# Optimization experiments

Hardware: AMD Instinct MI355X
Metric: run time of the kernel (lower is better)

The kernel has to match this reference:

```python
import jax, jax.numpy as jnp
import numpy as np
from jax import lax

EPS = 1e-5  # BatchNorm eps (torch default)


def _bn_relu_conv3x3_s2(x, bn_w, bn_b, bn_m, bn_v, w, b):
    # eval-mode BatchNorm2d -> ReLU -> conv3x3 stride 2 pad 1 (NCHW)
    inv = bn_w / jnp.sqrt(bn_v + EPS)
    y = x * inv[None, :, None, None] + (bn_b - bn_m * inv)[None, :, None, None]
    y = jax.nn.relu(y)
    y = lax.conv_general_dilated(y, w, window_strides=(2, 2),
                                 padding=((1, 1), (1, 1)),
                                 dimension_numbers=("NCHW", "OIHW", "NCHW"))
    return y + b[None, :, None, None]


def _avgpool2x2(x):
    B, C, H, W = x.shape
    return x.reshape(B, C, H // 2, 2, W // 2, 2).mean(axis=(3, 5))


def setup_inputs() -> dict:
    key = jax.random.key(0)
    ks = jax.random.split(key, 24)
    C, C3 = 128, 128 // 3
    d = {"x": jax.random.normal(ks[0], (8, C, 96, 96), jnp.float32)}
    for i, p in enumerate(["f", "g", "h"]):
        base = 1 + i * 6
        d[p + "_bn_w"] = jax.random.uniform(ks[base], (C,), jnp.float32, 0.5, 1.5)
        d[p + "_bn_b"] = jax.random.normal(ks[base + 1], (C,), jnp.float32) * 0.1
        d[p + "_bn_m"] = jax.random.normal(ks[base + 2], (C,), jnp.float32) * 0.1
        d[p + "_bn_v"] = jax.random.uniform(ks[base + 3], (C,), jnp.float32, 0.5, 1.5)
        d[p + "_w"] = jax.random.normal(ks[base + 4], (C, C, 3, 3), jnp.float32) * (1.0 / np.sqrt(9 * C))
        d[p + "_b"] = jax.random.normal(ks[base + 5], (C,), jnp.float32) * 0.01
    d["se_cw"] = jax.random.normal(ks[19], (C3, 2 * C), jnp.float32) * (1.0 / np.sqrt(2 * C))
    d["se_cb"] = jax.random.normal(ks[20], (C3,), jnp.float32) * 0.01
    d["se_uw"] = jax.random.normal(ks[21], (C, C3), jnp.float32) * (1.0 / np.sqrt(C3))
    d["se_ub"] = jax.random.normal(ks[22], (C,), jnp.float32) * 0.01
    d["gamma"] = jax.random.normal(ks[23], (1,), jnp.float32) * 0.5
    return d


def reference(x, f_bn_w, f_bn_b, f_bn_m, f_bn_v, f_w, f_b,
              g_bn_w, g_bn_b, g_bn_m, g_bn_v, g_w, g_b,
              h_bn_w, h_bn_b, h_bn_m, h_bn_v, h_w, h_b,
              se_cw, se_cb, se_uw, se_ub, gamma):
    B, C, H, W = x.shape
    left = _avgpool2x2(x)  # isPrimary=False branch -> [B,C,H/2,W/2]

    f = _bn_relu_conv3x3_s2(x, f_bn_w, f_bn_b, f_bn_m, f_bn_v, f_w, f_b)
    g = _bn_relu_conv3x3_s2(x, g_bn_w, g_bn_b, g_bn_m, g_bn_v, g_w, g_b)
    h = _bn_relu_conv3x3_s2(x, h_bn_w, h_bn_b, h_bn_m, h_bn_v, h_w, h_b)

    Ho, Wo = f.shape[2], f.shape[3]
    N = Ho * Wo
    ff = f.reshape(B, C, N)
    gg = g.reshape(B, C, N)
    hh = h.reshape(B, C, N)

    # s = softmax over last axis of f^T g : [B, N, N]
    scores = jnp.einsum("bcn,bcm->bnm", ff, gg)
    attn = jax.nn.softmax(scores, axis=2)
    s = jnp.einsum("bcn,bnm->bcm", hh, attn).reshape(B, C, Ho, Wo)
    s = gamma[0] * s

    # CompetitiveSE: global-avg x and s -> concat(2C) -> ReLU/1x1(C//3) -> ReLU/1x1(C)
    wx = x.mean(axis=(2, 3))          # [B, C]
    ws = s.mean(axis=(2, 3))          # [B, C]
    wcat = jnp.concatenate([wx, ws], axis=1)  # [B, 2C]
    se = jax.nn.relu(wcat) @ se_cw.T + se_cb
    se = jax.nn.relu(se) @ se_uw.T + se_ub    # [B, C]

    return (left + s) * (1.0 + se[:, :, None, None])
```

## Files before the change

kernel.cpp:

```cpp
#include <hip/hip_runtime.h>
#include <hip/hip_bf16.h>

#define B_   8
#define C_   128
#define H_   96
#define W_   96
#define HP_  98
#define HO_  48
#define N_   2304
#define K_CONV 1152
#define PLANE_IN  9216
#define TOT_OUT (B_*C_*N_)

typedef __attribute__((ext_vector_type(8))) short          s16x8;
typedef __attribute__((ext_vector_type(8))) unsigned short u16x8;
typedef __attribute__((ext_vector_type(4))) unsigned short u16x4;
typedef __attribute__((ext_vector_type(4))) float          f32x4;

#define SW(row, q)   (((row) << 6) + ((((q) ^ (((row) >> 1) & 3))) << 4))
#define SW8(row, q)  (((row) << 7) + ((((q) ^ ((row) & 7))) << 4))
#define SW16(row, q) (((row) << 8) + ((((q) ^ ((row) & 15))) << 4))

__device__ __forceinline__ ushort f2bf(float f) {
  __hip_bfloat16 h = __float2bfloat16(f);
  return *reinterpret_cast<ushort*>(&h);
}

__device__ __forceinline__ float block_reduce_sum_256(float v) {
  #pragma unroll
  for (int o = 32; o > 0; o >>= 1) v += __shfl_down(v, o, 64);
  __shared__ float r[4];
  int lane = threadIdx.x & 63, wv = threadIdx.x >> 6;
  if (lane == 0) r[wv] = v;
  __syncthreads();
  float s = 0.f;
  if (threadIdx.x == 0) s = r[0] + r[1] + r[2] + r[3];
  __syncthreads();
  return s;
}

__global__ void k_prep(const float* __restrict__ w0, const float* __restrict__ b0,
                       const float* __restrict__ m0, const float* __restrict__ v0,
                       const float* __restrict__ w1, const float* __restrict__ b1,
                       const float* __restrict__ m1, const float* __restrict__ v1,
                       const float* __restrict__ w2, const float* __restrict__ b2,
                       const float* __restrict__ m2, const float* __restrict__ v2,
                       float* __restrict__ inv, float* __restrict__ beta) {
  int p = blockIdx.x, c = threadIdx.x;
  const float* w = (p == 0 ? w0 : p == 1 ? w1 : w2);
  const float* bb = (p == 0 ? b0 : p == 1 ? b1 : b2);
  const float* m = (p == 0 ? m0 : p == 1 ? m1 : m2);
  const float* v = (p == 0 ? v0 : p == 1 ? v1 : v2);
  if (c < C_) {
    float iv = w[c] / sqrtf(v[c] + 1e-5f);
    inv[p * 128 + c] = iv;
    beta[p * 128 + c] = bb[c] - m[c] * iv;
  }
}

__global__ __launch_bounds__(256) void k_prep_w(const float* __restrict__ w0,
                                                const float* __restrict__ w1,
                                                const float* __restrict__ w2,
                                                ushort* __restrict__ o0,
                                                ushort* __restrict__ o1,
                                                ushort* __restrict__ o2) {
  int p = blockIdx.y;
  const float* w = (p == 0 ? w0 : p == 1 ? w1 : w2);
  ushort* wb = (p == 0 ? o0 : p == 1 ? o1 : o2);
  int id = blockIdx.x * 256 + threadIdx.x;
  if (id >= C_ * K_CONV) return;
  int co = id / K_CONV, rem = id - co * K_CONV;
  int tap = rem >> 7, ci = rem & 127;
  wb[id] = f2bf(w[co * K_CONV + ci * 9 + tap]);
}

__global__ __launch_bounds__(256) void k_prep_y(const float* __restrict__ x,
                                                const float* __restrict__ pinv,
                                                const float* __restrict__ pbeta,
                                                ushort* __restrict__ y0,
                                                ushort* __restrict__ y1,
                                                ushort* __restrict__ y2) {
  const int h1 = blockIdx.x, b = blockIdx.y, t = threadIdx.x;
  ushort* ys[3] = {y0 + (size_t)b * HP_ * HP_ * C_,
                   y1 + (size_t)b * HP_ * HP_ * C_,
                   y2 + (size_t)b * HP_ * HP_ * C_};
  u16x8 zer = (u16x8)0;
  if (h1 == 0 || h1 == HP_ - 1) {
    for (int p = 0; p < 3; ++p)
      for (int g = t; g < HP_ * C_ / 8; g += 256)
        *(u16x8*)(ys[p] + (size_t)h1 * HP_ * C_ + g * 8) = zer;
    return;
  }
  __shared__ float xs[128][97];
  const int h = h1 - 1;
  const float* xb = x + (size_t)b * C_ * PLANE_IN + h * W_;
  for (int id = t; id < 128 * 24; id += 256) {
    int ci = id / 24, w4 = id - ci * 24;
    float4 v = *(const float4*)(xb + (size_t)ci * PLANE_IN + w4 * 4);
    xs[ci][w4 * 4 + 0] = v.x; xs[ci][w4 * 4 + 1] = v.y;
    xs[ci][w4 * 4 + 2] = v.z; xs[ci][w4 * 4 + 3] = v.w;
  }
  __syncthreads();
  if (t < 32) {
    int side = t >> 4, cg = t & 15;
    for (int p = 0; p < 3; ++p)
      *(u16x8*)(ys[p] + ((size_t)h1 * HP_ + (side ? HP_ - 1 : 0)) * C_ + cg * 8) = zer;
  }
  for (int p = 0; p < 3; ++p) {
    const float* inv = pinv + p * 128;
    const float* bet = pbeta + p * 128;
    for (int g = t; g < 96 * 16; g += 256) {
      int wdx = g >> 4, cg = g & 15;
      u16x8 o;
      #pragma unroll
      for (int k = 0; k < 8; ++k) {
        int ci = cg * 8 + k;
        o[k] = f2bf(fmaxf(xs[ci][wdx] * inv[ci] + bet[ci], 0.f));
      }
      *(u16x8*)(ys[p] + ((size_t)h1 * HP_ + (wdx + 1)) * C_ + cg * 8) = o;
    }
  }
}

__global__ __launch_bounds__(256) void k_meanx(const float* __restrict__ x,
                                               float* __restrict__ wcat) {
  int bc = blockIdx.x;
  const float* p = x + (size_t)bc * PLANE_IN;
  float s = 0.f;
  for (int i = threadIdx.x; i < PLANE_IN; i += 256) s += p[i];
  s = block_reduce_sum_256(s);
  if (threadIdx.x == 0) {
    int b = bc >> 7, c = bc & 127;
    wcat[b * 256 + c] = fmaxf(s * (1.f / PLANE_IN), 0.f);
  }
}

__global__ __launch_bounds__(256) void k_conv3(
    const ushort* __restrict__ y0, const ushort* __restrict__ y1, const ushort* __restrict__ y2,
    const ushort* __restrict__ w0, const ushort* __restrict__ w1, const ushort* __restrict__ w2,
    const float* __restrict__ bi0, const float* __restrict__ bi1, const float* __restrict__ bi2,
    ushort* __restrict__ fo, ushort* __restrict__ go, ushort* __restrict__ ho) {
  __shared__ __align__(16) char smem[16384];
  char* As = smem;
  char* Bs = smem + 8192;
  const int br = blockIdx.y, b = blockIdx.z, n0 = blockIdx.x * 64;
  const int t = threadIdx.x, l = t & 63, w = t >> 6;
  const ushort* yb = (br == 0 ? y0 : br == 1 ? y1 : y2) + (size_t)b * HP_ * HP_ * C_;
  const ushort* wb = (br == 0 ? w0 : br == 1 ? w1 : w2);
  const float* bias = (br == 0 ? bi0 : br == 1 ? bi1 : bi2);
  const int pos = t >> 2, q = t & 3;
  const int n_glob = n0 + pos;
  const int oh = n_glob / HO_, ow = n_glob - oh * HO_;
  const int mh = (w & 1) * 64, nh = (w >> 1) * 32;
  f32x4 acc[4][2];
  #pragma unroll
  for (int i = 0; i < 4; ++i)
    #pragma unroll
    for (int j = 0; j < 2; ++j) acc[i][j] = (f32x4)0.f;

  for (int k0 = 0; k0 < K_CONV; k0 += 32) {
    int tap = k0 >> 7, ci0 = k0 & 127;
    int kh = tap / 3, kw = tap - kh * 3;
    #pragma unroll
    for (int g2 = 0; g2 < 2; ++g2) {
      int g = t + g2 * 256, row = g >> 2, qq = g & 3;
      u16x8 d = *(const u16x8*)(wb + row * K_CONV + k0 + qq * 8);
      *(u16x8*)(As + SW(row, qq)) = d;
    }
    {
      int h1 = 2 * oh + kh, w1 = 2 * ow + kw;
      u16x8 d = *(const u16x8*)(yb + ((size_t)h1 * HP_ + w1) * C_ + ci0 + q * 8);
      *(u16x8*)(Bs + SW(pos, q)) = d;
    }
    __syncthreads();
    s16x8 af[4], bf[2];
    #pragma unroll
    for (int i = 0; i < 4; ++i) {
      int r = mh + i * 16 + (l & 15);
      af[i] = *(const s16x8*)(As + SW(r, (l >> 4)));
    }
    #pragma unroll
    for (int j = 0; j < 2; ++j) {
      int r = nh + j * 16 + (l & 15);
      bf[j] = *(const s16x8*)(Bs + SW(r, (l >> 4)));
    }
    #pragma unroll
    for (int i = 0; i < 4; ++i)
      #pragma unroll
      for (int j = 0; j < 2; ++j)
        acc[i][j] = __builtin_amdgcn_mfma_f32_16x16x32_bf16(af[i], bf[j], acc[i][j], 0, 0, 0);
    __syncthreads();
  }

  if (br < 2) {
    ushort* out = (br == 0) ? fo : go;
    ushort* tb = (ushort*)smem;
    #pragma unroll
    for (int i = 0; i < 4; ++i) {
      int co4 = mh + i * 16 + (l >> 4) * 4;
      float4 bi = *(const float4*)&bias[co4];
      float bia[4] = {bi.x, bi.y, bi.z, bi.w};
      #pragma unroll
      for (int j = 0; j < 2; ++j) {
        int pp = nh + j * 16 + (l & 15);
        #pragma unroll
        for (int r = 0; r < 4; ++r)
          tb[pp * 128 + co4 + r] = f2bf(acc[i][j][r] + bia[r]);
      }
    }
    __syncthreads();
    #pragma unroll
    for (int it = 0; it < 4; ++it) {
      int g = t + it * 256;
      int row = g >> 4, gg = g & 15;
      u16x8 d = *(const u16x8*)(tb + row * 128 + gg * 8);
      *(u16x8*)(out + ((size_t)b * N_ + n0 + row) * C_ + gg * 8) = d;
    }
  } else {
    ushort* tb = (ushort*)smem;
    #pragma unroll
    for (int i = 0; i < 4; ++i) {
      int co4 = mh + i * 16 + (l >> 4) * 4;
      float4 bi = *(const float4*)&bias[co4];
      float bia[4] = {bi.x, bi.y, bi.z, bi.w};
      #pragma unroll
      for (int j = 0; j < 2; ++j) {
        int pp = nh + j * 16 + (l & 15);
        #pragma unroll
        for (int r = 0; r < 4; ++r)
          tb[(co4 + r) * 64 + pp] = f2bf(acc[i][j][r] + bia[r]);
      }
    }
    __syncthreads();
    for (int g = t; g < 1024; g += 256) {
      int co = g >> 3, off2 = (g & 7) * 8;
      u16x8 d = *(const u16x8*)(tb + co * 64 + off2);
      *(u16x8*)(ho + ((size_t)b * C_ + co) * N_ + n0 + off2) = d;
    }
  }
}

__global__ __launch_bounds__(256) void k_stats(const ushort* __restrict__ f,
                                               const ushort* __restrict__ g,
                                               float2* __restrict__ pstats) {
  __shared__ __align__(16) char smem[32768];
  char* fs = smem;
  char* gs = smem + 16384;
  const int blk = blockIdx.x;
  const int b = blk & 7, t2 = blk >> 3;
  const int n0 = (t2 % 36) * 64, mz = t2 / 36;
  const int t = threadIdx.x, l = t & 63, w = t >> 6, lo = l & 15, quad = l >> 4;
  const ushort* fb = f + (size_t)b * N_ * C_;
  const ushort* gb = g + (size_t)b * N_ * C_;
  #pragma unroll
  for (int it = 0; it < 4; ++it) {
    int G = t + it * 256, row = G >> 4, g16 = G & 15;
    *(u16x8*)(fs + SW16(row, g16)) = *(const u16x8*)(fb + (size_t)(n0 + row) * C_ + g16 * 8);
  }
  __syncthreads();
  s16x8 af[4];
  #pragma unroll
  for (int ks = 0; ks < 4; ++ks)
    af[ks] = *(const s16x8*)(fs + SW16(w * 16 + lo, ks * 4 + quad));
  float mloc[4], lloc[4];
  #pragma unroll
  for (int r = 0; r < 4; ++r) { mloc[r] = -1e30f; lloc[r] = 0.f; }
  const int m_beg = mz * 576;

  for (int i9 = 0; i9 < 9; ++i9) {
    int m0 = m_beg + i9 * 64;
    __syncthreads();
    #pragma unroll
    for (int it = 0; it < 4; ++it) {
      int G = t + it * 256, row = G >> 4, g16 = G & 15;
      *(u16x8*)(gs + SW16(row, g16)) = *(const u16x8*)(gb + (size_t)(m0 + row) * C_ + g16 * 8);
    }
    __syncthreads();
    f32x4 acc[4];
    #pragma unroll
    for (int j = 0; j < 4; ++j) acc[j] = (f32x4)0.f;
    #pragma unroll
    for (int ks = 0; ks < 4; ++ks)
      #pragma unroll
      for (int j = 0; j < 4; ++j) {
        s16x8 bf = *(const s16x8*)(gs + SW16(j * 16 + lo, ks * 4 + quad));
        acc[j] = __builtin_amdgcn_mfma_f32_16x16x32_bf16(af[ks], bf, acc[j], 0, 0, 0);
      }
    #pragma unroll
    for (int r = 0; r < 4; ++r) {
      float vmax = fmaxf(fmaxf(acc[0][r], acc[1][r]), fmaxf(acc[2][r], acc[3][r]));
      float mn = fmaxf(mloc[r], vmax);
      lloc[r] = lloc[r] * __expf(mloc[r] - mn) +
                __expf(acc[0][r] - mn) + __expf(acc[1][r] - mn) +
                __expf(acc[2][r] - mn) + __expf(acc[3][r] - mn);
      mloc[r] = mn;
    }
  }
  #pragma unroll
  for (int r = 0; r < 4; ++r) {
    #pragma unroll
    for (int o = 1; o < 16; o <<= 1) {
      float mo = __shfl_xor(mloc[r], o, 64);
      float lo2 = __shfl_xor(lloc[r], o, 64);
      float mn = fmaxf(mloc[r], mo);
      lloc[r] = lloc[r] * __expf(mloc[r] - mn) + lo2 * __expf(mo - mn);
      mloc[r] = mn;
    }
  }
  if (lo == 0) {
    #pragma unroll
    for (int r = 0; r < 4; ++r)
      pstats[((size_t)mz * B_ + b) * N_ + n0 + w * 16 + quad * 4 + r] =
          make_float2(mloc[r], lloc[r]);
  }
}

__global__ __launch_bounds__(256) void k_stats_red(const float2* __restrict__ p,
                                                   float2* __restrict__ stats) {
  int idx = blockIdx.x * 256 + threadIdx.x;
  if (idx >= B_ * N_) return;
  float mx = -1e30f, ls = 0.f;
  #pragma unroll
  for (int z = 0; z < 4; ++z) {
    float2 s = p[(size_t)z * B_ * N_ + idx];
    float mn = fmaxf(mx, s.x);
    ls = ls * __expf(mx - mn) + s.y * __expf(s.x - mn);
    mx = mn;
  }
  stats[idx] = make_float2(mx, ls);
}

__global__ __launch_bounds__(256) void k_attn_out(const ushort* __restrict__ f,
                                                  const ushort* __restrict__ g,
                                                  const ushort* __restrict__ h,
                                                  const float2* __restrict__ stats,
                                                  float* __restrict__ spart) {
  __shared__ __align__(16) char smem[35072];
  char* gs = smem;
  char* pTb = smem + 16384;
  const int blk = blockIdx.x;
  const int b = blk & 7, t2 = blk >> 3;
  const int m0 = (t2 % 36) * 64, nz = t2 / 36;
  const int t = threadIdx.x, l = t & 63, w = t >> 6, lo = l & 15, quad = l >> 4;
  const ushort* fb = f + (size_t)b * N_ * C_;
  const ushort* gb = g + (size_t)b * N_ * C_;
  const ushort* hb = h + (size_t)b * C_ * N_;
  const float2* stb = stats + (size_t)b * N_;
  #pragma unroll
  for (int it = 0; it < 4; ++it) {
    int G = t + it * 256, row = G >> 4, g16 = G & 15;
    *(u16x8*)(gs + SW16(row, g16)) = *(const u16x8*)(gb + (size_t)(m0 + row) * C_ + g16 * 8);
  }
  __syncthreads();
  f32x4 accs[2][4];
  #pragma unroll
  for (int i = 0; i < 2; ++i)
    #pragma unroll
    for (int j = 0; j < 4; ++j) accs[i][j] = (f32x4)0.f;
  const int n_beg = nz * 576;

  for (int i9 = 0; i9 < 9; ++i9) {
    int nb = n_beg + i9 * 64;
    char* pT = pTb + ((i9 & 1) << 13);
    s16x8 af[4], ah[2][2];
    #pragma unroll
    for (int ks = 0; ks < 4; ++ks)
      af[ks] = *(const s16x8*)(fb + (size_t)(nb + w * 16 + lo) * C_ + (ks * 4 + quad) * 8);
    #pragma unroll
    for (int i = 0; i < 2; ++i)
      #pragma unroll
      for (int ks = 0; ks < 2; ++ks)
        ah[i][ks] = *(const s16x8*)(hb + (size_t)((2 * w + i) * 16 + lo) * N_ + nb + (ks * 4 + quad) * 8);
    f32x4 sc[4];
    #pragma unroll
    for (int j = 0; j < 4; ++j) sc[j] = (f32x4)0.f;
    #pragma unroll
    for (int ks = 0; ks < 4; ++ks)
      #pragma unroll
      for (int j = 0; j < 4; ++j) {
        s16x8 bg = *(const s16x8*)(gs + SW16(j * 16 + lo, ks * 4 + quad));
        sc[j] = __builtin_amdgcn_mfma_f32_16x16x32_bf16(af[ks], bg, sc[j], 0, 0, 0);
      }
    float mxr[4], ilr[4];
    #pragma unroll
    for (int r = 0; r < 4; ++r) {
      float2 st = stb[nb + w * 16 + quad * 4 + r];
      mxr[r] = st.x; ilr[r] = 1.f / st.y;
    }
    const int nl = w * 16 + quad * 4;
    #pragma unroll
    for (int j = 0; j < 4; ++j) {
      u16x4 pv;
      #pragma unroll
      for (int r = 0; r < 4; ++r)
        pv[r] = f2bf(__expf(sc[j][r] - mxr[r]) * ilr[r]);
      *(u16x4*)(pT + SW8(j * 16 + lo, nl >> 3) + (nl & 7) * 2) = pv;
    }
    __syncthreads();
    #pragma unroll
    for (int ks = 0; ks < 2; ++ks)
      #pragma unroll
      for (int j = 0; j < 4; ++j) {
        s16x8 bp = *(const s16x8*)(pT + SW8(j * 16 + lo, ks * 4 + quad));
        accs[0][j] = __builtin_amdgcn_mfma_f32_16x16x32_bf16(ah[0][ks], bp, accs[0][j], 0, 0, 0);
        accs[1][j] = __builtin_amdgcn_mfma_f32_16x16x32_bf16(ah[1][ks], bp, accs[1][j], 0, 0, 0);
      }
  }
  __syncthreads();
  float* ss = (float*)smem;
  #pragma unroll
  for (int i = 0; i < 2; ++i) {
    int c0 = (2 * w + i) * 16 + quad * 4;
    #pragma unroll
    for (int j = 0; j < 4; ++j) {
      int m = j * 16 + lo;
      #pragma unroll
      for (int r = 0; r < 4; ++r)
        ss[(c0 + r) * 68 + m] = accs[i][j][r];
    }
  }
  __syncthreads();
  float* outp = spart + (size_t)nz * TOT_OUT + (size_t)b * C_ * N_ + m0;
  #pragma unroll
  for (int it = 0; it < 8; ++it) {
    int idx = t + it * 256;
    int c = idx >> 4, mq = idx & 15;
    float4 v = *(const float4*)&ss[c * 68 + mq * 4];
    *(float4*)&outp[(size_t)c * N_ + mq * 4] = v;
  }
}

__global__ __launch_bounds__(256) void k_sred(const float* __restrict__ spart,
                                              const float* __restrict__ gammap,
                                              float* __restrict__ sbuf) {
  int idx = blockIdx.x * 256 + threadIdx.x;
  if (idx >= TOT_OUT) return;
  float s = spart[idx] + spart[(size_t)TOT_OUT + idx] +
            spart[2 * (size_t)TOT_OUT + idx] + spart[3 * (size_t)TOT_OUT + idx];
  sbuf[idx] = gammap[0] * s;
}

__global__ __launch_bounds__(256) void k_means(const float* __restrict__ s,
                                               float* __restrict__ wcat) {
  int bc = blockIdx.x;
  const float* p = s + (size_t)bc * N_;
  float sm = 0.f;
  for (int i = threadIdx.x; i < N_; i += 256) sm += p[i];
  sm = block_reduce_sum_256(sm);
  if (threadIdx.x == 0) {
    int b = bc >> 7, c = bc & 127;
    wcat[b * 256 + 128 + c] = fmaxf(sm * (1.f / N_), 0.f);
  }
}

__global__ __launch_bounds__(128) void k_se(const float* __restrict__ wcat,
                                            const float* __restrict__ cw,
                                            const float* __restrict__ cb,
                                            const float* __restrict__ uw,
                                            const float* __restrict__ ub,
                                            float* __restrict__ se) {
  const int b = blockIdx.x, t = threadIdx.x;
  __shared__ float wc[256];
  __shared__ float s1[42];
  wc[t] = wcat[b * 256 + t];
  wc[128 + t] = wcat[b * 256 + 128 + t];
  __syncthreads();
  if (t < 42) {
    float a = cb[t];
    const float* r = cw + (size_t)t * 256;
    for (int k = 0; k < 256; ++k) a += wc[k] * r[k];
    s1[t] = fmaxf(a, 0.f);
  }
  __syncthreads();
  {
    float a = ub[t];
    const float* r = uw + (size_t)t * 42;
    for (int j = 0; j < 42; ++j) a += s1[j] * r[j];
    se[b * 128 + t] = a;
  }
}

__global__ __launch_bounds__(256) void k_final(const float* __restrict__ x,
                                               const float* __restrict__ s,
                                               const float* __restrict__ se,
                                               float* __restrict__ out) {
  int idx = blockIdx.x * 256 + threadIdx.x;
  if (idx >= TOT_OUT) return;
  int m  = idx % N_;
  int bc = idx / N_;
  int oh = m / HO_, ow = m - oh * HO_;
  const float* xp = x + (size_t)bc * PLANE_IN;
  int ih = oh * 2, iw = ow * 2;
  float l = 0.25f * (xp[ih * W_ + iw] + xp[ih * W_ + iw + 1] +
                     xp[(ih + 1) * W_ + iw] + xp[(ih + 1) * W_ + iw + 1]);
  out[idx] = (l + s[idx]) * (1.f + se[bc]);
}

extern "C" void kernel_launch(void* const* d_in, const int* in_sizes, int n_in,
                              void* d_out, int out_size, void* d_ws, size_t ws_size,
                              hipStream_t stream) {
  (void)in_sizes; (void)n_in; (void)out_size; (void)ws_size;
  const float* x    = (const float*)d_in[0];
  const float* bnw[3] = {(const float*)d_in[1],  (const float*)d_in[7],  (const float*)d_in[13]};
  const float* bnb[3] = {(const float*)d_in[2],  (const float*)d_in[8],  (const float*)d_in[14]};
  const float* bnm[3] = {(const float*)d_in[3],  (const float*)d_in[9],  (const float*)d_in[15]};
  const float* bnv[3] = {(const float*)d_in[4],  (const float*)d_in[10], (const float*)d_in[16]};
  const float* cw_[3] = {(const float*)d_in[5],  (const float*)d_in[11], (const float*)d_in[17]};
  const float* cbb[3] = {(const float*)d_in[6],  (const float*)d_in[12], (const float*)d_in[18]};
  const float* secw = (const float*)d_in[19];
  const float* secb = (const float*)d_in[20];
  const float* seuw = (const float*)d_in[21];
  const float* seub = (const float*)d_in[22];
  const float* gamma = (const float*)d_in[23];
  float* out = (float*)d_out;

  char* ws = (char*)d_ws;
  size_t off = 0;
  auto alloc = [&](size_t bytes) -> char* {
    char* p = ws + off;
    off = (off + bytes + 255) & ~(size_t)255;
    return p;
  };
  ushort* yp[3];
  for (int p = 0; p < 3; ++p) yp[p] = (ushort*)alloc((size_t)B_ * HP_ * HP_ * C_ * 2);
  ushort* wb[3];
  for (int p = 0; p < 3; ++p) wb[p] = (ushort*)alloc((size_t)C_ * K_CONV * 2);
  ushort* fbuf = (ushort*)alloc((size_t)B_ * N_ * C_ * 2);
  ushort* gbuf = (ushort*)alloc((size_t)B_ * N_ * C_ * 2);
  ushort* hbuf = (ushort*)alloc((size_t)B_ * C_ * N_ * 2);
  float2* pstats = (float2*)alloc((size_t)4 * B_ * N_ * 8);
  float2* stats  = (float2*)alloc((size_t)B_ * N_ * 8);
  float*  spart = (float*)alloc((size_t)4 * TOT_OUT * 4);
  float*  sbuf = (float*)alloc((size_t)TOT_OUT * 4);
  float*  wcat = (float*)alloc(B_ * 256 * 4);
  float*  sebuf = (float*)alloc(B_ * 128 * 4);
  float*  pinv  = (float*)alloc(3 * 128 * 4);
  float*  pbeta = (float*)alloc(3 * 128 * 4);

  k_prep<<<3, 128, 0, stream>>>(bnw[0], bnb[0], bnm[0], bnv[0],
                                bnw[1], bnb[1], bnm[1], bnv[1],
                                bnw[2], bnb[2], bnm[2], bnv[2], pinv, pbeta);
  k_prep_w<<<dim3((C_ * K_CONV + 255) / 256, 3), 256, 0, stream>>>(
      cw_[0], cw_[1], cw_[2], wb[0], wb[1], wb[2]);
  k_prep_y<<<dim3(HP_, B_), 256, 0, stream>>>(x, pinv, pbeta, yp[0], yp[1], yp[2]);
  k_meanx<<<B_ * C_, 256, 0, stream>>>(x, wcat);

  k_conv3<<<dim3(N_ / 64, 3, B_), 256, 0, stream>>>(yp[0], yp[1], yp[2],
                                                    wb[0], wb[1], wb[2],
                                                    cbb[0], cbb[1], cbb[2],
                                                    fbuf, gbuf, hbuf);

  k_stats<<<1152, 256, 0, stream>>>(fbuf, gbuf, pstats);
  k_stats_red<<<(B_ * N_ + 255) / 256, 256, 0, stream>>>(pstats, stats);
  k_attn_out<<<1152, 256, 0, stream>>>(fbuf, gbuf, hbuf, stats, spart);
  k_sred<<<(TOT_OUT + 255) / 256, 256, 0, stream>>>(spart, gamma, sbuf);

  k_means<<<B_ * C_, 256, 0, stream>>>(sbuf, wcat);
  k_se<<<B_, 128, 0, stream>>>(wcat, secw, secb, seuw, seub, sebuf);

  k_final<<<(TOT_OUT + 255) / 256, 256, 0, stream>>>(x, sbuf, sebuf, out);
}
```

Measured before the change: 301.9 us.

## Drop LDS staging in stats and attention kernels, add MFMA priority hints

```diff
diff --git a/kernel.cpp b/kernel.cpp
--- a/kernel.cpp
+++ b/kernel.cpp
@@ -240,52 +240,38 @@
   }
 }
 
-__global__ __launch_bounds__(256) void k_stats(const ushort* __restrict__ f,
-                                               const ushort* __restrict__ g,
-                                               float2* __restrict__ pstats) {
-  __shared__ __align__(16) char smem[32768];
-  char* fs = smem;
-  char* gs = smem + 16384;
+__global__ __launch_bounds__(256, 6) void k_stats(const ushort* __restrict__ f,
+                                                  const ushort* __restrict__ g,
+                                                  float2* __restrict__ pstats) {
   const int blk = blockIdx.x;
   const int b = blk & 7, t2 = blk >> 3;
   const int n0 = (t2 % 36) * 64, mz = t2 / 36;
   const int t = threadIdx.x, l = t & 63, w = t >> 6, lo = l & 15, quad = l >> 4;
   const ushort* fb = f + (size_t)b * N_ * C_;
   const ushort* gb = g + (size_t)b * N_ * C_;
-  #pragma unroll
-  for (int it = 0; it < 4; ++it) {
-    int G = t + it * 256, row = G >> 4, g16 = G & 15;
-    *(u16x8*)(fs + SW16(row, g16)) = *(const u16x8*)(fb + (size_t)(n0 + row) * C_ + g16 * 8);
-  }
-  __syncthreads();
   s16x8 af[4];
   #pragma unroll
   for (int ks = 0; ks < 4; ++ks)
-    af[ks] = *(const s16x8*)(fs + SW16(w * 16 + lo, ks * 4 + quad));
+    af[ks] = *(const s16x8*)(fb + (size_t)(n0 + w * 16 + lo) * C_ + (ks * 4 + quad) * 8);
   float mloc[4], lloc[4];
   #pragma unroll
   for (int r = 0; r < 4; ++r) { mloc[r] = -1e30f; lloc[r] = 0.f; }
   const int m_beg = mz * 576;
 
   for (int i9 = 0; i9 < 9; ++i9) {
-    int m0 = m_beg + i9 * 64;
-    __syncthreads();
-    #pragma unroll
-    for (int it = 0; it < 4; ++it) {
-      int G = t + it * 256, row = G >> 4, g16 = G & 15;
-      *(u16x8*)(gs + SW16(row, g16)) = *(const u16x8*)(gb + (size_t)(m0 + row) * C_ + g16 * 8);
-    }
-    __syncthreads();
+    const ushort* gp = gb + (size_t)(m_beg + i9 * 64) * C_;
     f32x4 acc[4];
     #pragma unroll
     for (int j = 0; j < 4; ++j) acc[j] = (f32x4)0.f;
+    __builtin_amdgcn_s_setprio(1);
     #pragma unroll
     for (int ks = 0; ks < 4; ++ks)
       #pragma unroll
       for (int j = 0; j < 4; ++j) {
-        s16x8 bf = *(const s16x8*)(gs + SW16(j * 16 + lo, ks * 4 + quad));
+        s16x8 bf = *(const s16x8*)(gp + (size_t)(j * 16 + lo) * C_ + (ks * 4 + quad) * 8);
         acc[j] = __builtin_amdgcn_mfma_f32_16x16x32_bf16(af[ks], bf, acc[j], 0, 0, 0);
       }
+    __builtin_amdgcn_s_setprio(0);
     #pragma unroll
     for (int r = 0; r < 4; ++r) {
       float vmax = fmaxf(fmaxf(acc[0][r], acc[1][r]), fmaxf(acc[2][r], acc[3][r]));
@@ -330,12 +316,12 @@
   stats[idx] = make_float2(mx, ls);
 }
 
-__global__ __launch_bounds__(256) void k_attn_out(const ushort* __restrict__ f,
-                                                  const ushort* __restrict__ g,
-                                                  const ushort* __restrict__ h,
-                                                  const float2* __restrict__ stats,
-                                                  float* __restrict__ spart) {
-  __shared__ __align__(16) char smem[35072];
+__global__ __launch_bounds__(256, 5) void k_attn_out(const ushort* __restrict__ f,
+                                                     const ushort* __restrict__ g,
+                                                     const ushort* __restrict__ h,
+                                                     const float2* __restrict__ stats,
+                                                     float* __restrict__ spart) {
+  __shared__ __align__(16) char smem[32768];
   char* gs = smem;
   char* pTb = smem + 16384;
   const int blk = blockIdx.x;
@@ -371,9 +357,16 @@
       #pragma unroll
       for (int ks = 0; ks < 2; ++ks)
         ah[i][ks] = *(const s16x8*)(hb + (size_t)((2 * w + i) * 16 + lo) * N_ + nb + (ks * 4 + quad) * 8);
+    float mxr[4], ilr[4];
+    #pragma unroll
+    for (int r = 0; r < 4; ++r) {
+      float2 st = stb[nb + w * 16 + quad * 4 + r];
+      mxr[r] = st.x; ilr[r] = 1.f / st.y;
+    }
     f32x4 sc[4];
     #pragma unroll
     for (int j = 0; j < 4; ++j) sc[j] = (f32x4)0.f;
+    __builtin_amdgcn_s_setprio(1);
     #pragma unroll
     for (int ks = 0; ks < 4; ++ks)
       #pragma unroll
@@ -381,12 +374,7 @@
         s16x8 bg = *(const s16x8*)(gs + SW16(j * 16 + lo, ks * 4 + quad));
         sc[j] = __builtin_amdgcn_mfma_f32_16x16x32_bf16(af[ks], bg, sc[j], 0, 0, 0);
       }
-    float mxr[4], ilr[4];
-    #pragma unroll
-    for (int r = 0; r < 4; ++r) {
-      float2 st = stb[nb + w * 16 + quad * 4 + r];
-      mxr[r] = st.x; ilr[r] = 1.f / st.y;
-    }
+    __builtin_amdgcn_s_setprio(0);
     const int nl = w * 16 + quad * 4;
     #pragma unroll
     for (int j = 0; j < 4; ++j) {
@@ -397,6 +385,7 @@
       *(u16x4*)(pT + SW8(j * 16 + lo, nl >> 3) + (nl & 7) * 2) = pv;
     }
     __syncthreads();
+    __builtin_amdgcn_s_setprio(1);
     #pragma unroll
     for (int ks = 0; ks < 2; ++ks)
       #pragma unroll
@@ -405,9 +394,9 @@
         accs[0][j] = __builtin_amdgcn_mfma_f32_16x16x32_bf16(ah[0][ks], bp, accs[0][j], 0, 0, 0);
         accs[1][j] = __builtin_amdgcn_mfma_f32_16x16x32_bf16(ah[1][ks], bp, accs[1][j], 0, 0, 0);
       }
-  }
-  __syncthreads();
-  float* ss = (float*)smem;
+    __builtin_amdgcn_s_setprio(0);
+  }
+  float* outp = spart + (size_t)nz * TOT_OUT + (size_t)b * C_ * N_ + m0;
   #pragma unroll
   for (int i = 0; i < 2; ++i) {
     int c0 = (2 * w + i) * 16 + quad * 4;
@@ -416,17 +405,8 @@
       int m = j * 16 + lo;
       #pragma unroll
       for (int r = 0; r < 4; ++r)
-        ss[(c0 + r) * 68 + m] = accs[i][j][r];
-    }
-  }
-  __syncthreads();
-  float* outp = spart + (size_t)nz * TOT_OUT + (size_t)b * C_ * N_ + m0;
-  #pragma unroll
-  for (int it = 0; it < 8; ++it) {
-    int idx = t + it * 256;
-    int c = idx >> 4, mq = idx & 15;
-    float4 v = *(const float4*)&ss[c * 68 + mq * 4];
-    *(float4*)&outp[(size_t)c * N_ + mq * 4] = v;
+        outp[(size_t)(c0 + r) * N_ + m] = accs[i][j][r];
+    }
   }
 }
 
```

After: 382.4 us. 26.7% more time.
